# Kernel optimization log

Measured on AMD Instinct MI355X. Metric: run time of the kernel, lower is better.

## Reference

```python
import jax, jax.numpy as jnp
import numpy as np
from jax import lax

WS = 7          # window size
SHIFT = 3       # shift size
HEADS = 16
DIM = 512
NREF = 100
H_IMG = 112
W_IMG = 112
BATCH = 2
HD = DIM // HEADS
SCALE = HD ** (-0.5)
EPS = 1e-5


def _layernorm(x, w, b):
    mu = jnp.mean(x, axis=-1, keepdims=True)
    var = jnp.mean((x - mu) ** 2, axis=-1, keepdims=True)
    return (x - mu) / jnp.sqrt(var + EPS) * w + b


def _rel_pos_index():
    coords = np.stack(np.meshgrid(np.arange(WS), np.arange(WS), indexing='ij'))  # (2,ws,ws)
    cf = coords.reshape(2, -1)
    rel = cf[:, :, None] - cf[:, None, :]
    rel = rel.transpose(1, 2, 0).astype(np.int64)
    rel[..., 0] += WS - 1
    rel[..., 1] += WS - 1
    rel[..., 0] *= 2 * WS - 1
    return rel.sum(-1).reshape(-1)  # (N*N,)

_RPI = _rel_pos_index()


def setup_inputs() -> dict:
    key = jax.random.key(0)
    ks = jax.random.split(key, 16)
    C = DIM
    s = 0.02
    x = jax.random.normal(ks[0], (BATCH, H_IMG * W_IMG, C), jnp.float32)
    x_ref = jax.random.normal(ks[1], (BATCH, NREF, C), jnp.float32)
    # shifted-window attention mask (standard Swin construction)
    img = np.zeros((H_IMG, W_IMG))
    cnt = 0
    for hs in (slice(0, -WS), slice(-WS, -SHIFT), slice(-SHIFT, None)):
        for ws_ in (slice(0, -WS), slice(-WS, -SHIFT), slice(-SHIFT, None)):
            img[hs, ws_] = cnt
            cnt += 1
    mw = img.reshape(H_IMG // WS, WS, W_IMG // WS, WS).transpose(0, 2, 1, 3).reshape(-1, WS * WS)
    am = mw[:, None, :] - mw[:, :, None]
    mask = jnp.asarray(np.where(am != 0, -100.0, 0.0), jnp.float32)  # (nW, N, N)
    return dict(
        x=x, x_ref=x_ref, mask=mask,
        norm1_w=jnp.ones((C,), jnp.float32), norm1_b=jnp.zeros((C,), jnp.float32),
        qkv_w=jax.random.normal(ks[2], (3 * C, C), jnp.float32) * s,
        qkv_b=jnp.zeros((3 * C,), jnp.float32),
        diff_mu=jax.random.normal(ks[3], (1, 1, C), jnp.float32),
        diff_logsigma=jax.random.normal(ks[4], (1, 1, C), jnp.float32) * s,
        rpb_table=jax.random.normal(ks[5], ((2 * WS - 1) ** 2, HEADS), jnp.float32) * s,
        ref_qk_w=jax.random.normal(ks[6], (2 * C, C), jnp.float32) * s,
        ref_qk_b=jnp.zeros((2 * C,), jnp.float32),
        conv_w=jax.random.normal(ks[7], (HEADS, HEADS, 3, 3), jnp.float32) * s,
        conv_b=jnp.zeros((HEADS,), jnp.float32),
        proj_w=jax.random.normal(ks[8], (C, C), jnp.float32) * s,
        proj_b=jnp.zeros((C,), jnp.float32),
        norm2_w=jnp.ones((C,), jnp.float32), norm2_b=jnp.zeros((C,), jnp.float32),
        fc1_w=jax.random.normal(ks[9], (4 * C, C), jnp.float32) * s,
        fc1_b=jnp.zeros((4 * C,), jnp.float32),
        fc2_w=jax.random.normal(ks[10], (C, 4 * C), jnp.float32) * s,
        fc2_b=jnp.zeros((C,), jnp.float32),
        Hh=H_IMG, Ww=W_IMG,
    )


def _window_attention(xw, mask, x_ref, qkv_w, qkv_b, diff_mu, diff_logsigma,
                      rpb_table, ref_qk_w, ref_qk_b, conv_w, conv_b, proj_w, proj_b):
    B_, N, C = xw.shape
    rB = x_ref.shape[0]
    n_win = B_ // rB
    qkv = (xw @ qkv_w.T + qkv_b).reshape(B_, N, 3, HEADS, HD).transpose(2, 0, 3, 1, 4)
    q, k, v = qkv[0], qkv[1], qkv[2]  # (B_, heads, N, hd)
    # reference tokens -> q/v with reparameterized shift/scale
    ref_qk = (x_ref @ ref_qk_w.T + ref_qk_b).reshape(rB, NREF, 2, C).transpose(2, 0, 1, 3)
    ref_q = diff_mu + jnp.exp(diff_logsigma) * ref_qk[0]
    ref_q = ref_q.reshape(rB, NREF, HEADS, HD).transpose(0, 2, 1, 3)
    ref_v = ref_qk[1].reshape(rB, NREF, HEADS, HD).transpose(0, 2, 1, 3)
    ref_k = jnp.repeat(ref_q, n_win, axis=0)  # (B_, heads, nref, hd)
    ref_v = jnp.repeat(ref_v, n_win, axis=0)
    ra = jnp.einsum('bhnd,bhrd->bhnr', q, ref_k)  # (B_, heads, N, nref)
    ra = ra.reshape(rB, n_win, HEADS, N, NREF).transpose(0, 2, 1, 3, 4).reshape(rB, HEADS, n_win * N, NREF)
    # 3 rounds of conv diffusion + layernorm(no affine) + gelu, residual
    for _ in range(3):
        u = lax.conv_general_dilated(ra, conv_w, (1, 1), 'SAME',
                                     dimension_numbers=('NCHW', 'OIHW', 'NCHW'))
        u = u + conv_b[None, :, None, None]
        mu = jnp.mean(u, axis=(-2, -1), keepdims=True)
        var = jnp.mean((u - mu) ** 2, axis=(-2, -1), keepdims=True)
        u = jax.nn.gelu((u - mu) / jnp.sqrt(var + EPS), approximate=False)
        ra = ra + u
    ra = ra.reshape(rB, HEADS, n_win, N, NREF).transpose(0, 2, 1, 3, 4).reshape(B_, HEADS, N, NREF)
    ra = jax.nn.softmax(ra, axis=-1)
    q_new = jnp.einsum('bhnr,bhrd->bhnd', ra, ref_v) * SCALE
    attn = jnp.einsum('bhnd,bhmd->bhnm', q_new, k)
    rpb = rpb_table[_RPI].reshape(N, N, HEADS).transpose(2, 0, 1)  # (heads, N, N)
    attn = attn + rpb[None]
    nW = mask.shape[0]
    attn = attn.reshape(B_ // nW, nW, HEADS, N, N) + mask[None, :, None]
    attn = jax.nn.softmax(attn.reshape(B_, HEADS, N, N), axis=-1)
    out = jnp.einsum('bhnm,bhmd->bhnd', attn, v).transpose(0, 2, 1, 3).reshape(B_, N, C)
    return out @ proj_w.T + proj_b


def reference(x, x_ref, mask, norm1_w, norm1_b, qkv_w, qkv_b, diff_mu, diff_logsigma,
              rpb_table, ref_qk_w, ref_qk_b, conv_w, conv_b, proj_w, proj_b,
              norm2_w, norm2_b, fc1_w, fc1_b, fc2_w, fc2_b, Hh, Ww):
    B, L, C = x.shape
    shortcut = x
    xn = _layernorm(x, norm1_w, norm1_b).reshape(B, Hh, Ww, C)
    # cyclic shift
    sx = jnp.roll(xn, (-SHIFT, -SHIFT), axis=(1, 2))
    # window partition -> (B*nWin, ws*ws, C)
    xw = sx.reshape(B, Hh // WS, WS, Ww // WS, WS, C).transpose(0, 1, 3, 2, 4, 5).reshape(-1, WS * WS, C)
    aw = _window_attention(xw, mask, x_ref, qkv_w, qkv_b, diff_mu, diff_logsigma,
                           rpb_table, ref_qk_w, ref_qk_b, conv_w, conv_b, proj_w, proj_b)
    # window reverse
    sx = aw.reshape(B, Hh // WS, Ww // WS, WS, WS, C).transpose(0, 1, 3, 2, 4, 5).reshape(B, Hh, Ww, C)
    xn = jnp.roll(sx, (SHIFT, SHIFT), axis=(1, 2)).reshape(B, L, C)
    x = shortcut + xn
    h = _layernorm(x, norm2_w, norm2_b)
    h = jax.nn.gelu(h @ fc1_w.T + fc1_b, approximate=False)
    return x + (h @ fc2_w.T + fc2_b)
```

## Files before the change

### kernel.cpp

```cpp
#include <hip/hip_runtime.h>
#include <hip/hip_bf16.h>

typedef __attribute__((ext_vector_type(8))) short short8;
typedef __attribute__((ext_vector_type(8))) unsigned short ushort8;
typedef __attribute__((ext_vector_type(4))) float f32x4;
typedef __attribute__((ext_vector_type(4))) unsigned int u32x4;
typedef __attribute__((ext_vector_type(2))) unsigned int u32x2;

#define DEV __device__ __forceinline__

DEV float gelu_f(float x) { return 0.5f * x * (1.f + erff(x * 0.70710678118654752440f)); }

DEV float bf2f(unsigned short s) {
  unsigned int t = ((unsigned int)s) << 16;
  float f; __builtin_memcpy(&f, &t, 4); return f;
}
DEV unsigned short f2bf(float f) {
  __hip_bfloat16 b = __float2bfloat16(f);
  unsigned short s; __builtin_memcpy(&s, &b, 2); return s;
}

DEV void async_copy16(void* lds, const void* g) {
  __builtin_amdgcn_global_load_lds(
      (const __attribute__((address_space(1))) unsigned int*)g,
      (__attribute__((address_space(3))) unsigned int*)lds, 16, 0, 0);
}

DEV void block_reduce2(float& s, float& s2) {
  __shared__ float red[8];
  int tid = threadIdx.x;
#pragma unroll
  for (int o = 32; o > 0; o >>= 1) { s += __shfl_down(s, o); s2 += __shfl_down(s2, o); }
  if ((tid & 63) == 0) { red[tid >> 6] = s; red[4 + (tid >> 6)] = s2; }
  __syncthreads();
  s  = red[0] + red[1] + red[2] + red[3];
  s2 = red[4] + red[5] + red[6] + red[7];
}

__global__ __launch_bounds__(256) void f2b_kernel(const float* __restrict__ in,
                                                  __hip_bfloat16* __restrict__ o, int n) {
  int i = blockIdx.x * 256 + threadIdx.x;
  if (i < n) o[i] = __float2bfloat16(in[i]);
}

__global__ __launch_bounds__(256) void maskb_kernel(const float* __restrict__ mask,
                                                    unsigned short* __restrict__ maskB) {
  int i = blockIdx.x * 256 + threadIdx.x;
  int m = i % 56, rest = i / 56;
  int n = rest % 49, win = rest / 49;
  unsigned short v = 0;
  if (m < 49) v = f2bf(mask[((size_t)win * 49 + n) * 49 + m]);
  maskB[i] = v;
}

__global__ __launch_bounds__(256) void rpbt_kernel(const float* __restrict__ rpb,
                                                   unsigned short* __restrict__ rpbT) {
  int i = blockIdx.x * 256 + threadIdx.x;
  if (i >= 43904) return;
  int m = i % 56, rest = i / 56;
  int n = rest % 49, h = rest / 49;
  unsigned short v = 0;
  if (m < 49) {
    int rp = (n / 7 - m / 7 + 6) * 13 + (n % 7 - m % 7 + 6);
    v = f2bf(rpb[rp * 16 + h]);
  }
  rpbT[i] = v;
}

__global__ __launch_bounds__(256) void ln1_window_kernel(
    const float* __restrict__ x, const float* __restrict__ w, const float* __restrict__ b,
    __hip_bfloat16* __restrict__ xw) {
  int t = blockIdx.x;
  int b_ = t / 49, n = t % 49;
  int bb = b_ >> 8, win = b_ & 255;
  int wi = win >> 4, wj = win & 15;
  int ii = n / 7, jj = n % 7;
  int sh = (wi * 7 + ii + 3) % 112;
  int sw = (wj * 7 + jj + 3) % 112;
  const float* row = x + ((size_t)bb * 12544 + sh * 112 + sw) * 512;
  int tid = threadIdx.x;
  float v0 = row[tid], v1 = row[tid + 256];
  float s = v0 + v1, s2 = v0 * v0 + v1 * v1;
  block_reduce2(s, s2);
  float mu = s * (1.f / 512.f);
  float rstd = rsqrtf(s2 * (1.f / 512.f) - mu * mu + 1e-5f);
  __hip_bfloat16* orow = xw + (size_t)t * 512;
  orow[tid]       = __float2bfloat16((v0 - mu) * rstd * w[tid] + b[tid]);
  orow[tid + 256] = __float2bfloat16((v1 - mu) * rstd * w[tid + 256] + b[tid + 256]);
}

template <int EPI>
__global__ __launch_bounds__(256) void gemm_bt(
    const __hip_bfloat16* __restrict__ A, const __hip_bfloat16* __restrict__ B,
    const float* __restrict__ bias, float* __restrict__ outF,
    __hip_bfloat16* __restrict__ outB, int M, int N, int K) {
  __shared__ __align__(16) __hip_bfloat16 As[128 * 64];
  __shared__ __align__(16) __hip_bfloat16 Bs[128 * 64];
  int m0 = blockIdx.x * 128, n0 = blockIdx.y * 128;
  int tid = threadIdx.x;
  int wave = tid >> 6, lane = tid & 63;
  int wm = (wave & 1) * 64, wn = (wave >> 1) * 64;
  int lrow = lane & 15, kq = lane >> 4;
  int srow = lane >> 3, scol = (lane & 7) * 8;
  f32x4 acc[4][4] = {};
  for (int k0 = 0; k0 < K; k0 += 64) {
    int rb = wave * 32;
#pragma unroll
    for (int i = 0; i < 4; i++) {
      int row = rb + i * 8 + srow;
      async_copy16(&As[(rb + i * 8) * 64], &A[(size_t)(m0 + row) * K + k0 + scol]);
      async_copy16(&Bs[(rb + i * 8) * 64], &B[(size_t)(n0 + row) * K + k0 + scol]);
    }
    __syncthreads();
#pragma unroll
    for (int ks = 0; ks < 2; ks++) {
      short8 af[4], bf[4];
#pragma unroll
      for (int t = 0; t < 4; t++) {
        af[t] = *reinterpret_cast<const short8*>(&As[(wm + t * 16 + lrow) * 64 + ks * 32 + kq * 8]);
        bf[t] = *reinterpret_cast<const short8*>(&Bs[(wn + t * 16 + lrow) * 64 + ks * 32 + kq * 8]);
      }
#pragma unroll
      for (int tm = 0; tm < 4; tm++)
#pragma unroll
        for (int tn = 0; tn < 4; tn++)
          acc[tm][tn] = __builtin_amdgcn_mfma_f32_16x16x32_bf16(af[tm], bf[tn], acc[tm][tn], 0, 0, 0);
    }
    __syncthreads();
  }
#pragma unroll
  for (int tm = 0; tm < 4; tm++) {
#pragma unroll
    for (int tn = 0; tn < 4; tn++) {
      int col = n0 + wn + tn * 16 + lrow;
      float bv = bias[col];
#pragma unroll
      for (int r = 0; r < 4; r++) {
        int row = m0 + wm + tm * 16 + kq * 4 + r;
        float v = acc[tm][tn][r] + bv;
        size_t o = (size_t)row * N + col;
        if (EPI == 1) outB[o] = __float2bfloat16(v);
        else if (EPI == 2) outB[o] = __float2bfloat16(gelu_f(v));
        else outF[o] += v;
      }
    }
  }
}

__global__ __launch_bounds__(256) void ref_kernel(
    const float* __restrict__ x_ref, const float* __restrict__ w, const float* __restrict__ bias,
    const float* __restrict__ diff_mu, const float* __restrict__ diff_ls,
    unsigned short* __restrict__ refq, unsigned short* __restrict__ refvT) {
  int blk = blockIdx.x;
  int b = blk / 100, r = blk % 100;
  __shared__ float xs[512];
  int tid = threadIdx.x;
  const float* xr = x_ref + (size_t)(b * 100 + r) * 512;
  xs[tid] = xr[tid];
  xs[tid + 256] = xr[tid + 256];
  __syncthreads();
#pragma unroll
  for (int cc = 0; cc < 4; cc++) {
    int c = cc * 256 + tid;
    const float* wr = w + (size_t)c * 512;
    float s = bias[c];
    for (int k = 0; k < 512; k++) s += xs[k] * wr[k];
    if (c < 512) {
      float v = diff_mu[c] + expf(diff_ls[c]) * s;
      int hh = c >> 5, d = c & 31;
      refq[((size_t)(b * 16 + hh) * 100 + r) * 32 + d] = f2bf(v);
    } else {
      int c2 = c - 512, hh = c2 >> 5, d = c2 & 31;
      refvT[(((size_t)b * 16 + hh) * 32 + d) * 100 + r] = f2bf(s);
    }
  }
}

__global__ __launch_bounds__(256) void ra_kernel(
    const __hip_bfloat16* __restrict__ q, const unsigned short* __restrict__ refq,
    __hip_bfloat16* __restrict__ ra) {
  __shared__ __align__(16) unsigned short q_s[64 * 40];
  __shared__ __align__(16) unsigned short rq_s[112 * 40];
  int blk = blockIdx.x;
  int b_ = blk >> 4, h = blk & 15;
  int rb = b_ >> 8, win = b_ & 255;
  int tid = threadIdx.x;
  int wave = tid >> 6, lane = tid & 63;
  int lrow = lane & 15, kq = lane >> 4;
  u32x4 z4 = {};
  const unsigned short* qb = (const unsigned short*)q + (size_t)b_ * 49 * 512 + h * 32;
  for (int i = tid; i < 196; i += 256) {
    int n = i >> 2, c = i & 3;
    *reinterpret_cast<u32x4*>(&q_s[n * 40 + c * 8]) =
        *reinterpret_cast<const u32x4*>(&qb[n * 512 + c * 8]);
  }
  for (int i = tid; i < 60; i += 256) {
    int n = 49 + (i >> 2), c = i & 3;
    *reinterpret_cast<u32x4*>(&q_s[n * 40 + c * 8]) = z4;
  }
  const unsigned short* rqg = refq + (size_t)(rb * 16 + h) * 3200;
  for (int i = tid; i < 400; i += 256) {
    int r = i >> 2, c = i & 3;
    *reinterpret_cast<u32x4*>(&rq_s[r * 40 + c * 8]) =
        *reinterpret_cast<const u32x4*>(&rqg[r * 32 + c * 8]);
  }
  for (int i = tid; i < 48; i += 256) {
    int r = 100 + (i >> 2), c = i & 3;
    *reinterpret_cast<u32x4*>(&rq_s[r * 40 + c * 8]) = z4;
  }
  __syncthreads();
  short8 a = *reinterpret_cast<const short8*>(&q_s[(wave * 16 + lrow) * 40 + kq * 8]);
  unsigned short* ra_base = (unsigned short*)ra + ((size_t)(rb * 16 + h) * 12544 + win * 49) * 100;
  f32x4 zero = {};
#pragma unroll
  for (int nt = 0; nt < 7; nt++) {
    short8 b = *reinterpret_cast<const short8*>(&rq_s[(nt * 16 + lrow) * 40 + kq * 8]);
    f32x4 c = __builtin_amdgcn_mfma_f32_16x16x32_bf16(a, b, zero, 0, 0, 0);
    int col = nt * 16 + lrow;
#pragma unroll
    for (int r = 0; r < 4; r++) {
      int n = wave * 16 + kq * 4 + r;
      if (n < 49 && col < 100) ra_base[n * 100 + col] = f2bf(c[r]);
    }
  }
}

__global__ __launch_bounds__(256) void conv_kernel(
    const __hip_bfloat16* __restrict__ ra_, const float* __restrict__ cw, const float* __restrict__ cb,
    __hip_bfloat16* __restrict__ u_, float* __restrict__ psum, float* __restrict__ psumsq) {
  __shared__ __align__(16) unsigned short in_s[6 * 103 * 24];
  __shared__ __align__(16) unsigned short w_s[16 * 160];
  __shared__ float sred_s[4][16], sred_s2[4][16];
  const unsigned short* ra = (const unsigned short*)ra_;
  unsigned short* u = (unsigned short*)u_;
  int yt = blockIdx.x, bb = blockIdx.y;
  int y0 = yt * 4;
  int tid = threadIdx.x;
  int wave = tid >> 6, lane = tid & 63;
  int lrow = lane & 15, kq = lane >> 4;
  for (int i = tid; i < 2560; i += 256) {
    int co = i / 160, k = i % 160;
    unsigned short v = 0;
    if (k < 144) {
      int ci = k & 15, p = k >> 4;
      v = f2bf(cw[(co * 16 + ci) * 9 + p]);
    }
    w_s[i] = v;
  }
  for (int i = tid; i < 288; i += 256) {
    int ci = i & 15, rem = i >> 4;
    int yl = rem / 3, xs = rem % 3;
    int xl = (xs == 0) ? 0 : (100 + xs);
    in_s[(yl * 103 + xl) * 24 + ci] = 0;
  }
  if (tid < 192) {
    int unit = tid >> 1, par = tid & 1;
    int ci = unit / 6, yl = unit % 6;
    int gy = y0 - 1 + yl;
    bool rv = (gy >= 0 && gy < 12544);
    const unsigned short* rp = ra + (((size_t)bb * 16 + ci) * 12544 + (rv ? gy : 0)) * 100;
    unsigned short* lp = &in_s[(yl * 103 + 1) * 24 + ci];
#pragma unroll 4
    for (int c = par; c < 25; c += 2) {
      u32x2 d = {0u, 0u};
      if (rv) d = *reinterpret_cast<const u32x2*>(&rp[c * 4]);
      lp[(c * 4 + 0) * 24] = (unsigned short)(d[0] & 0xffff);
      lp[(c * 4 + 1) * 24] = (unsigned short)(d[0] >> 16);
      lp[(c * 4 + 2) * 24] = (unsigned short)(d[1] & 0xffff);
      lp[(c * 4 + 3) * 24] = (unsigned short)(d[1] >> 16);
    }
  }
  __syncthreads();

  short8 afr[5];
#pragma unroll
  for (int c = 0; c < 5; c++)
    afr[c] = *reinterpret_cast<const short8*>(&w_s[lrow * 160 + c * 32 + kq * 8]);
  int kqh = kq >> 1, ci0 = (kq & 1) * 8;
  int kyA[5], kxA[5];
#pragma unroll
  for (int c = 0; c < 5; c++) {
    int p = c * 2 + kqh; if (p > 8) p = 0;
    kyA[c] = p / 3; kxA[c] = p % 3;
  }
  float bias_r[4];
#pragma unroll
  for (int r = 0; r < 4; r++) bias_r[r] = cb[kq * 4 + r];
  float s_r[4] = {0.f, 0.f, 0.f, 0.f}, s2_r[4] = {0.f, 0.f, 0.f, 0.f};

  int yl = wave;
  int gy = y0 + yl;
#pragma unroll
  for (int xg = 0; xg < 7; xg++) {
    int px = xg * 16 + lrow;
    int pxc = px < 100 ? px : 99;
    f32x4 acc = {};
#pragma unroll
    for (int c = 0; c < 5; c++) {
      short8 bfrag = *reinterpret_cast<const short8*>(
          &in_s[((yl + kyA[c]) * 103 + pxc + kxA[c]) * 24 + ci0]);
      acc = __builtin_amdgcn_mfma_f32_16x16x32_bf16(afr[c], bfrag, acc, 0, 0, 0);
    }
    bool valid = px < 100;
#pragma unroll
    for (int r = 0; r < 4; r++) {
      float v = acc[r] + bias_r[r];
      if (valid) {
        u[(((size_t)bb * 16 + kq * 4 + r) * 12544 + gy) * 100 + px] = f2bf(v);
        s_r[r] += v; s2_r[r] += v * v;
      }
    }
  }
#pragma unroll
  for (int o = 1; o < 16; o <<= 1)
#pragma unroll
    for (int r = 0; r < 4; r++) { s_r[r] += __shfl_xor(s_r[r], o); s2_r[r] += __shfl_xor(s2_r[r], o); }
  if (lrow == 0)
#pragma unroll
    for (int r = 0; r < 4; r++) { sred_s[wave][kq * 4 + r] = s_r[r]; sred_s2[wave][kq * 4 + r] = s2_r[r]; }
  __syncthreads();
  if (tid < 16) {
    float s  = sred_s[0][tid] + sred_s[1][tid] + sred_s[2][tid] + sred_s[3][tid];
    float s2 = sred_s2[0][tid] + sred_s2[1][tid] + sred_s2[2][tid] + sred_s2[3][tid];
    size_t pi = ((size_t)bb * 3136 + yt) * 16 + tid;
    psum[pi] = s; psumsq[pi] = s2;
  }
}

__global__ __launch_bounds__(256) void conv_stats_kernel(
    const float* __restrict__ psum, const float* __restrict__ psumsq, float* __restrict__ stats) {
  int g = blockIdx.x;
  int bb = g >> 4, co = g & 15;
  int tid = threadIdx.x;
  float s = 0.f, s2 = 0.f;
  for (int t = tid; t < 3136; t += 256) {
    size_t pi = ((size_t)bb * 3136 + t) * 16 + co;
    s += psum[pi];
    s2 += psumsq[pi];
  }
  block_reduce2(s, s2);
  if (tid == 0) {
    const float inv = 1.f / 1254400.f;
    float mu = s * inv;
    float var = s2 * inv - mu * mu;
    stats[g * 2] = mu;
    stats[g * 2 + 1] = rsqrtf(var + 1e-5f);
  }
}

__global__ __launch_bounds__(256) void conv_apply_kernel(
    __hip_bfloat16* __restrict__ ra, const __hip_bfloat16* __restrict__ u,
    const float* __restrict__ stats) {
  const int total8 = 5017600;
  int stride = gridDim.x * 256;
  for (int i = blockIdx.x * 256 + threadIdx.x; i < total8; i += stride) {
    int g = i / 156800;
    float mu = stats[g * 2], rstd = stats[g * 2 + 1];
    ushort8 uu = reinterpret_cast<const ushort8*>(u)[i];
    ushort8 rr = reinterpret_cast<const ushort8*>(ra)[i];
    ushort8 oo;
#pragma unroll
    for (int j = 0; j < 8; j++) {
      float rv = bf2f(rr[j]) + gelu_f((bf2f(uu[j]) - mu) * rstd);
      oo[j] = f2bf(rv);
    }
    reinterpret_cast<ushort8*>(ra)[i] = oo;
  }
}

__global__ __launch_bounds__(256) void attn_kernel(
    const __hip_bfloat16* __restrict__ ra_, const unsigned short* __restrict__ refvT,
    const __hip_bfloat16* __restrict__ kv_, const unsigned short* __restrict__ rpbT,
    const unsigned short* __restrict__ maskB, __hip_bfloat16* __restrict__ att_) {
  __shared__ __align__(16) char smem[36352];
  unsigned short* P1  = (unsigned short*)smem;
  unsigned short* rvT = (unsigned short*)(smem + 17408);
  unsigned short* P2  = (unsigned short*)smem;
  unsigned short* vT  = (unsigned short*)(smem + 9216);
  unsigned short* qn  = (unsigned short*)(smem + 26112);
  unsigned short* kb  = (unsigned short*)(smem + 31232);

  int blk = blockIdx.x;
  int b_ = blk >> 4, h = blk & 15;
  int rb = b_ >> 8, win = b_ & 255;
  int tid = threadIdx.x;
  int wave = tid >> 6, lane = tid & 63;
  int lrow = lane & 15, kq = lane >> 4;
  const unsigned short* ra = (const unsigned short*)ra_;
  const unsigned short* kv = (const unsigned short*)kv_;
  unsigned short* att = (unsigned short*)att_;
  u32x2 zz = {};

  const unsigned short* rab = ra + ((size_t)(rb * 16 + h) * 12544 + win * 49) * 100;
  for (int i = tid; i < 1225; i += 256) {
    int n = i / 25, c = i % 25;
    *reinterpret_cast<u32x2*>(&P1[n * 136 + c * 4]) =
        *reinterpret_cast<const u32x2*>(&rab[n * 100 + c * 4]);
  }
  for (int i = tid; i < 343; i += 256) {
    int n = i / 7, c = i % 7;
    *reinterpret_cast<u32x2*>(&P1[n * 136 + 100 + c * 4]) = zz;
  }
  const unsigned short* rvtg = refvT + (size_t)(rb * 16 + h) * 3200;
  for (int i = tid; i < 800; i += 256) {
    int d = i / 25, c = i % 25;
    *reinterpret_cast<u32x2*>(&rvT[d * 136 + c * 4]) =
        *reinterpret_cast<const u32x2*>(&rvtg[d * 100 + c * 4]);
  }
  for (int i = tid; i < 224; i += 256) {
    int d = i / 7, c = i % 7;
    *reinterpret_cast<u32x2*>(&rvT[d * 136 + 100 + c * 4]) = zz;
  }
  const unsigned short* kvb = kv + (size_t)b_ * 49 * 1024;
  for (int i = tid; i < 196; i += 256) {
    int m = i >> 2, c = i & 3;
    *reinterpret_cast<u32x4*>(&kb[m * 40 + c * 8]) =
        *reinterpret_cast<const u32x4*>(&kvb[m * 1024 + h * 32 + c * 8]);
  }
  __syncthreads();

  if (tid < 196) {
    int n = tid >> 2, q = tid & 3;
    unsigned short* row = P1 + n * 136;
    float mx = -1e30f;
    for (int r = q * 25; r < q * 25 + 25; r++) mx = fmaxf(mx, bf2f(row[r]));
    mx = fmaxf(mx, __shfl_xor(mx, 1));
    mx = fmaxf(mx, __shfl_xor(mx, 2));
    float sm = 0.f;
    for (int r = q * 25; r < q * 25 + 25; r++) {
      float e = __expf(bf2f(row[r]) - mx); sm += e; row[r] = f2bf(e);
    }
    sm += __shfl_xor(sm, 1);
    sm += __shfl_xor(sm, 2);
    float inv = 1.f / sm;
    for (int r = q * 25; r < q * 25 + 25; r++) row[r] = f2bf(bf2f(row[r]) * inv);
  }
  __syncthreads();

  f32x4 acc1[2] = {};
#pragma unroll
  for (int ks = 0; ks < 4; ks++) {
    short8 a = *reinterpret_cast<const short8*>(&P1[(wave * 16 + lrow) * 136 + ks * 32 + kq * 8]);
#pragma unroll
    for (int dt = 0; dt < 2; dt++) {
      short8 b = *reinterpret_cast<const short8*>(&rvT[(dt * 16 + lrow) * 136 + ks * 32 + kq * 8]);
      acc1[dt] = __builtin_amdgcn_mfma_f32_16x16x32_bf16(a, b, acc1[dt], 0, 0, 0);
    }
  }
#pragma unroll
  for (int dt = 0; dt < 2; dt++)
#pragma unroll
    for (int r = 0; r < 4; r++) {
      int n = wave * 16 + kq * 4 + r;
      qn[n * 40 + dt * 16 + lrow] = f2bf(acc1[dt][r] * 0.17677669529663688f);
    }
  __syncthreads();

  for (int i = tid; i < 196; i += 256) {
    int m = i >> 2, dg = (i & 3) * 8;
    ushort8 vv = *reinterpret_cast<const ushort8*>(&kvb[m * 1024 + 512 + h * 32 + dg]);
#pragma unroll
    for (int j = 0; j < 8; j++) vT[(dg + j) * 72 + m] = vv[j];
  }
  for (int i = tid; i < 480; i += 256) vT[(i / 15) * 72 + 49 + i % 15] = 0;

  const unsigned short* bt = maskB + (size_t)win * 2744;
  const unsigned short* rt = rpbT + (size_t)h * 2744;
  short8 aq = *reinterpret_cast<const short8*>(&qn[(wave * 16 + lrow) * 40 + kq * 8]);
  f32x4 zero = {};
  float val[4][4];
#pragma unroll
  for (int mt = 0; mt < 4; mt++) {
    short8 bk = *reinterpret_cast<const short8*>(&kb[(mt * 16 + lrow) * 40 + kq * 8]);
    f32x4 lg = __builtin_amdgcn_mfma_f32_16x16x32_bf16(aq, bk, zero, 0, 0, 0);
    int m = mt * 16 + lrow;
#pragma unroll
    for (int r = 0; r < 4; r++) {
      int n = wave * 16 + kq * 4 + r;
      float v;
      if (m < 49 && n < 49)
        v = lg[r] + bf2f(rt[n * 56 + m]) + bf2f(bt[n * 56 + m]);
      else v = -1e30f;
      val[mt][r] = v;
    }
  }
#pragma unroll
  for (int r = 0; r < 4; r++) {
    float mx = -1e30f;
#pragma unroll
    for (int mt = 0; mt < 4; mt++) mx = fmaxf(mx, val[mt][r]);
    mx = fmaxf(mx, __shfl_xor(mx, 1)); mx = fmaxf(mx, __shfl_xor(mx, 2));
    mx = fmaxf(mx, __shfl_xor(mx, 4)); mx = fmaxf(mx, __shfl_xor(mx, 8));
    float sm = 0.f, e[4];
#pragma unroll
    for (int mt = 0; mt < 4; mt++) { e[mt] = __expf(val[mt][r] - mx); sm += e[mt]; }
    sm += __shfl_xor(sm, 1); sm += __shfl_xor(sm, 2);
    sm += __shfl_xor(sm, 4); sm += __shfl_xor(sm, 8);
    float inv = 1.f / sm;
    int n = wave * 16 + kq * 4 + r;
#pragma unroll
    for (int mt = 0; mt < 4; mt++) P2[n * 72 + mt * 16 + lrow] = f2bf(e[mt] * inv);
  }
  __syncthreads();

  f32x4 acc2[2] = {};
#pragma unroll
  for (int ks = 0; ks < 2; ks++) {
    short8 ap = *reinterpret_cast<const short8*>(&P2[(wave * 16 + lrow) * 72 + ks * 32 + kq * 8]);
#pragma unroll
    for (int dt = 0; dt < 2; dt++) {
      short8 bv = *reinterpret_cast<const short8*>(&vT[(dt * 16 + lrow) * 72 + ks * 32 + kq * 8]);
      acc2[dt] = __builtin_amdgcn_mfma_f32_16x16x32_bf16(ap, bv, acc2[dt], 0, 0, 0);
    }
  }
  unsigned short* ab = att + (size_t)b_ * 49 * 512 + h * 32;
#pragma unroll
  for (int dt = 0; dt < 2; dt++)
#pragma unroll
    for (int r = 0; r < 4; r++) {
      int n = wave * 16 + kq * 4 + r;
      if (n < 49) ab[n * 512 + dt * 16 + lrow] = f2bf(acc2[dt][r]);
    }
}

__global__ __launch_bounds__(256) void resid_ln2_kernel(
    const float* __restrict__ x, const __hip_bfloat16* __restrict__ proj_out,
    const float* __restrict__ w2, const float* __restrict__ b2,
    float* __restrict__ out, __hip_bfloat16* __restrict__ hout) {
  int blk = blockIdx.x;
  int bb = blk / 12544, l = blk % 12544;
  int hh = l / 112, ww = l % 112;
  int hs = (hh + 109) % 112, wsx = (ww + 109) % 112;
  int t = (bb * 256 + (hs / 7) * 16 + (wsx / 7)) * 49 + (hs % 7) * 7 + (wsx % 7);
  const float* xr = x + (size_t)blk * 512;
  const __hip_bfloat16* pr = proj_out + (size_t)t * 512;
  int tid = threadIdx.x;
  float v0 = xr[tid] + __bfloat162float(pr[tid]);
  float v1 = xr[tid + 256] + __bfloat162float(pr[tid + 256]);
  float* orow = out + (size_t)blk * 512;
  orow[tid] = v0;
  orow[tid + 256] = v1;
  float s = v0 + v1, s2 = v0 * v0 + v1 * v1;
  block_reduce2(s, s2);
  float mu = s * (1.f / 512.f);
  float rstd = rsqrtf(s2 * (1.f / 512.f) - mu * mu + 1e-5f);
  __hip_bfloat16* hrow = hout + (size_t)blk * 512;
  hrow[tid]       = __float2bfloat16((v0 - mu) * rstd * w2[tid] + b2[tid]);
  hrow[tid + 256] = __float2bfloat16((v1 - mu) * rstd * w2[tid + 256] + b2[tid + 256]);
}

extern "C" void kernel_launch(void* const* d_in, const int* in_sizes, int n_in,
                              void* d_out, int out_size, void* d_ws, size_t ws_size,
                              hipStream_t stream) {
  const float* x       = (const float*)d_in[0];
  const float* x_ref   = (const float*)d_in[1];
  const float* mask    = (const float*)d_in[2];
  const float* n1w     = (const float*)d_in[3];
  const float* n1b     = (const float*)d_in[4];
  const float* qkv_w   = (const float*)d_in[5];
  const float* qkv_b   = (const float*)d_in[6];
  const float* diff_mu = (const float*)d_in[7];
  const float* diff_ls = (const float*)d_in[8];
  const float* rpb     = (const float*)d_in[9];
  const float* ref_w   = (const float*)d_in[10];
  const float* ref_b   = (const float*)d_in[11];
  const float* conv_w  = (const float*)d_in[12];
  const float* conv_b  = (const float*)d_in[13];
  const float* proj_w  = (const float*)d_in[14];
  const float* proj_b  = (const float*)d_in[15];
  const float* n2w     = (const float*)d_in[16];
  const float* n2b     = (const float*)d_in[17];
  const float* fc1_w   = (const float*)d_in[18];
  const float* fc1_b   = (const float*)d_in[19];
  const float* fc2_w   = (const float*)d_in[20];
  const float* fc2_b   = (const float*)d_in[21];
  float* out = (float*)d_out;

  char* ws = (char*)d_ws;
  size_t off = 0;
  auto alloc = [&](size_t bytes) -> char* {
    char* p = ws + off;
    off += (bytes + 255) & ~(size_t)255;
    return p;
  };
  __hip_bfloat16* wq_bf = (__hip_bfloat16*)alloc(1536ULL * 512 * 2);
  __hip_bfloat16* wp_bf = (__hip_bfloat16*)alloc(512ULL * 512 * 2);
  __hip_bfloat16* w1_bf = (__hip_bfloat16*)alloc(2048ULL * 512 * 2);
  __hip_bfloat16* w2_bf = (__hip_bfloat16*)alloc(512ULL * 2048 * 2);
  unsigned short* refq  = (unsigned short*)alloc(2ULL * 16 * 100 * 32 * 2);
  unsigned short* refvT = (unsigned short*)alloc(2ULL * 16 * 32 * 100 * 2);
  unsigned short* maskB = (unsigned short*)alloc(256ULL * 49 * 56 * 2);
  unsigned short* rpbT  = (unsigned short*)alloc(16ULL * 49 * 56 * 2);
  float* psum  = (float*)alloc(2ULL * 3136 * 16 * 4);
  float* psumq = (float*)alloc(2ULL * 3136 * 16 * 4);
  float* stats = (float*)alloc(64 * 4);
  char* regX  = alloc(25088ULL * 512 * 2);
  char* regQ  = alloc(25088ULL * 512 * 2);
  char* regRA = alloc(2ULL * 16 * 12544 * 100 * 2);
  char* regU  = alloc(2ULL * 16 * 12544 * 100 * 2);

  __hip_bfloat16* xw_bf   = (__hip_bfloat16*)regX;
  __hip_bfloat16* att_bf  = (__hip_bfloat16*)regX;
  __hip_bfloat16* q_bf    = (__hip_bfloat16*)regQ;
  __hip_bfloat16* h_bf    = (__hip_bfloat16*)regQ;
  __hip_bfloat16* ra      = (__hip_bfloat16*)regRA;
  __hip_bfloat16* hg      = (__hip_bfloat16*)regRA;
  __hip_bfloat16* u       = (__hip_bfloat16*)regU;
  __hip_bfloat16* kv_bf   = (__hip_bfloat16*)regU;
  __hip_bfloat16* proj_bf = (__hip_bfloat16*)(regU + 51380224);

  f2b_kernel<<<3072, 256, 0, stream>>>(qkv_w, wq_bf, 786432);
  f2b_kernel<<<1024, 256, 0, stream>>>(proj_w, wp_bf, 262144);
  f2b_kernel<<<4096, 256, 0, stream>>>(fc1_w, w1_bf, 1048576);
  f2b_kernel<<<4096, 256, 0, stream>>>(fc2_w, w2_bf, 1048576);
  maskb_kernel<<<2744, 256, 0, stream>>>(mask, maskB);
  rpbt_kernel<<<172, 256, 0, stream>>>(rpb, rpbT);
  ln1_window_kernel<<<25088, 256, 0, stream>>>(x, n1w, n1b, xw_bf);
  gemm_bt<1><<<dim3(196, 4), 256, 0, stream>>>(xw_bf, wq_bf, qkv_b, nullptr, q_bf,
                                               25088, 512, 512);
  ref_kernel<<<200, 256, 0, stream>>>(x_ref, ref_w, ref_b, diff_mu, diff_ls, refq, refvT);
  ra_kernel<<<8192, 256, 0, stream>>>(q_bf, refq, ra);
  for (int rd = 0; rd < 3; rd++) {
    conv_kernel<<<dim3(3136, 2), 256, 0, stream>>>(ra, conv_w, conv_b, u, psum, psumq);
    conv_stats_kernel<<<32, 256, 0, stream>>>(psum, psumq, stats);
    conv_apply_kernel<<<4096, 256, 0, stream>>>(ra, u, stats);
  }
  gemm_bt<1><<<dim3(196, 8), 256, 0, stream>>>(xw_bf, wq_bf + 512 * 512, qkv_b + 512,
                                               nullptr, kv_bf, 25088, 1024, 512);
  attn_kernel<<<8192, 256, 0, stream>>>(ra, refvT, kv_bf, rpbT, maskB, att_bf);
  gemm_bt<1><<<dim3(196, 4), 256, 0, stream>>>(att_bf, wp_bf, proj_b, nullptr, proj_bf,
                                               25088, 512, 512);
  resid_ln2_kernel<<<25088, 256, 0, stream>>>(x, proj_bf, n2w, n2b, out, h_bf);
  for (int ch = 0; ch < 2; ch++) {
    const __hip_bfloat16* hA = h_bf + (size_t)ch * 12544 * 512;
    gemm_bt<2><<<dim3(98, 16), 256, 0, stream>>>(hA, w1_bf, fc1_b, nullptr, hg,
                                                 12544, 2048, 512);
    gemm_bt<3><<<dim3(98, 4), 256, 0, stream>>>(hg, w2_bf, fc2_b,
                                                out + (size_t)ch * 12544 * 512, nullptr,
                                                12544, 512, 2048);
  }
}
```

Before: 1.187 ms.

## Fuse final conv residual-GELU into attention kernel and defer softmax normalization

The last conv_apply pass is skipped. Its residual plus GELU on the normalized conv output is instead computed inside the attention kernel as the ref-attention tile is loaded. Because u must stay live until then, kv gets its own buffer when the workspace is large enough, with the old aliasing kept as a fallback. The ref softmax now keeps values in registers and folds the 1/sum into the scale applied after the MFMA, which drops one LDS read-modify-write pass. The cost is an extra global read of u inside attention and more workspace memory.

Measured after the change: 1.185 ms. No clear change (-0.2%).

```diff
diff --git a/kernel.cpp b/kernel.cpp
--- a/kernel.cpp
+++ b/kernel.cpp
@@ -368,17 +368,20 @@
   }
 }
 
+template <int FUSE>
 __global__ __launch_bounds__(256) void attn_kernel(
-    const __hip_bfloat16* __restrict__ ra_, const unsigned short* __restrict__ refvT,
+    const __hip_bfloat16* __restrict__ ra_, const __hip_bfloat16* __restrict__ u_,
+    const float* __restrict__ stats, const unsigned short* __restrict__ refvT,
     const __hip_bfloat16* __restrict__ kv_, const unsigned short* __restrict__ rpbT,
     const unsigned short* __restrict__ maskB, __hip_bfloat16* __restrict__ att_) {
-  __shared__ __align__(16) char smem[36352];
+  __shared__ __align__(16) char smem[36608];
   unsigned short* P1  = (unsigned short*)smem;
   unsigned short* rvT = (unsigned short*)(smem + 17408);
   unsigned short* P2  = (unsigned short*)smem;
   unsigned short* vT  = (unsigned short*)(smem + 9216);
   unsigned short* qn  = (unsigned short*)(smem + 26112);
   unsigned short* kb  = (unsigned short*)(smem + 31232);
+  float* lsum         = (float*)(smem + 36352);
 
   int blk = blockIdx.x;
   int b_ = blk >> 4, h = blk & 15;
@@ -387,15 +390,38 @@
   int wave = tid >> 6, lane = tid & 63;
   int lrow = lane & 15, kq = lane >> 4;
   const unsigned short* ra = (const unsigned short*)ra_;
+  const unsigned short* ug = (const unsigned short*)u_;
   const unsigned short* kv = (const unsigned short*)kv_;
   unsigned short* att = (unsigned short*)att_;
   u32x2 zz = {};
 
-  const unsigned short* rab = ra + ((size_t)(rb * 16 + h) * 12544 + win * 49) * 100;
+  if (tid < 64) lsum[tid] = 1.0f;
+  float mu = 0.f, rstd = 0.f;
+  if (FUSE) { mu = stats[(rb * 16 + h) * 2]; rstd = stats[(rb * 16 + h) * 2 + 1]; }
+
+  const size_t tile_off = ((size_t)(rb * 16 + h) * 12544 + win * 49) * 100;
+  const unsigned short* rab = ra + tile_off;
+  const unsigned short* uab = ug + tile_off;
   for (int i = tid; i < 1225; i += 256) {
     int n = i / 25, c = i % 25;
-    *reinterpret_cast<u32x2*>(&P1[n * 136 + c * 4]) =
-        *reinterpret_cast<const u32x2*>(&rab[n * 100 + c * 4]);
+    u32x2 rv = *reinterpret_cast<const u32x2*>(&rab[n * 100 + c * 4]);
+    if (FUSE) {
+      u32x2 uv = *reinterpret_cast<const u32x2*>(&uab[n * 100 + c * 4]);
+      unsigned short rr4[4] = {(unsigned short)(rv[0] & 0xffff), (unsigned short)(rv[0] >> 16),
+                               (unsigned short)(rv[1] & 0xffff), (unsigned short)(rv[1] >> 16)};
+      unsigned short uu4[4] = {(unsigned short)(uv[0] & 0xffff), (unsigned short)(uv[0] >> 16),
+                               (unsigned short)(uv[1] & 0xffff), (unsigned short)(uv[1] >> 16)};
+      unsigned short o4[4];
+#pragma unroll
+      for (int j = 0; j < 4; j++)
+        o4[j] = f2bf(bf2f(rr4[j]) + gelu_f((bf2f(uu4[j]) - mu) * rstd));
+      u32x2 w;
+      w[0] = (unsigned int)o4[0] | ((unsigned int)o4[1] << 16);
+      w[1] = (unsigned int)o4[2] | ((unsigned int)o4[3] << 16);
+      *reinterpret_cast<u32x2*>(&P1[n * 136 + c * 4]) = w;
+    } else {
+      *reinterpret_cast<u32x2*>(&P1[n * 136 + c * 4]) = rv;
+    }
   }
   for (int i = tid; i < 343; i += 256) {
     int n = i / 7, c = i % 7;
@@ -421,19 +447,23 @@
 
   if (tid < 196) {
     int n = tid >> 2, q = tid & 3;
-    unsigned short* row = P1 + n * 136;
+    unsigned short* row = P1 + n * 136 + q * 25;
+    float e[25];
+#pragma unroll
+    for (int r = 0; r < 25; r++) e[r] = bf2f(row[r]);
     float mx = -1e30f;
-    for (int r = q * 25; r < q * 25 + 25; r++) mx = fmaxf(mx, bf2f(row[r]));
+#pragma unroll
+    for (int r = 0; r < 25; r++) mx = fmaxf(mx, e[r]);
     mx = fmaxf(mx, __shfl_xor(mx, 1));
     mx = fmaxf(mx, __shfl_xor(mx, 2));
     float sm = 0.f;
-    for (int r = q * 25; r < q * 25 + 25; r++) {
-      float e = __expf(bf2f(row[r]) - mx); sm += e; row[r] = f2bf(e);
-    }
+#pragma unroll
+    for (int r = 0; r < 25; r++) { e[r] = __expf(e[r] - mx); sm += e[r]; }
     sm += __shfl_xor(sm, 1);
     sm += __shfl_xor(sm, 2);
-    float inv = 1.f / sm;
-    for (int r = q * 25; r < q * 25 + 25; r++) row[r] = f2bf(bf2f(row[r]) * inv);
+#pragma unroll
+    for (int r = 0; r < 25; r++) row[r] = f2bf(e[r]);
+    if (q == 0) lsum[n] = sm;
   }
   __syncthreads();
 
@@ -447,12 +477,16 @@
       acc1[dt] = __builtin_amdgcn_mfma_f32_16x16x32_bf16(a, b, acc1[dt], 0, 0, 0);
     }
   }
+  float invl[4];
+#pragma unroll
+  for (int r = 0; r < 4; r++)
+    invl[r] = 0.17677669529663688f / lsum[wave * 16 + kq * 4 + r];
 #pragma unroll
   for (int dt = 0; dt < 2; dt++)
 #pragma unroll
     for (int r = 0; r < 4; r++) {
       int n = wave * 16 + kq * 4 + r;
-      qn[n * 40 + dt * 16 + lrow] = f2bf(acc1[dt][r] * 0.17677669529663688f);
+      qn[n * 40 + dt * 16 + lrow] = f2bf(acc1[dt][r] * invl[r]);
     }
   __syncthreads();
 
@@ -606,8 +640,12 @@
   __hip_bfloat16* ra      = (__hip_bfloat16*)regRA;
   __hip_bfloat16* hg      = (__hip_bfloat16*)regRA;
   __hip_bfloat16* u       = (__hip_bfloat16*)regU;
-  __hip_bfloat16* kv_bf   = (__hip_bfloat16*)regU;
   __hip_bfloat16* proj_bf = (__hip_bfloat16*)(regU + 51380224);
+
+  const size_t kv_bytes = 25088ULL * 1024 * 2;
+  bool fused = (ws_size >= off + kv_bytes);
+  __hip_bfloat16* kv_bf = fused ? (__hip_bfloat16*)alloc(kv_bytes)
+                                : (__hip_bfloat16*)regU;
 
   f2b_kernel<<<3072, 256, 0, stream>>>(qkv_w, wq_bf, 786432);
   f2b_kernel<<<1024, 256, 0, stream>>>(proj_w, wp_bf, 262144);
@@ -623,11 +661,15 @@
   for (int rd = 0; rd < 3; rd++) {
     conv_kernel<<<dim3(3136, 2), 256, 0, stream>>>(ra, conv_w, conv_b, u, psum, psumq);
     conv_stats_kernel<<<32, 256, 0, stream>>>(psum, psumq, stats);
-    conv_apply_kernel<<<4096, 256, 0, stream>>>(ra, u, stats);
+    if (rd < 2 || !fused)
+      conv_apply_kernel<<<4096, 256, 0, stream>>>(ra, u, stats);
   }
   gemm_bt<1><<<dim3(196, 8), 256, 0, stream>>>(xw_bf, wq_bf + 512 * 512, qkv_b + 512,
                                                nullptr, kv_bf, 25088, 1024, 512);
-  attn_kernel<<<8192, 256, 0, stream>>>(ra, refvT, kv_bf, rpbT, maskB, att_bf);
+  if (fused)
+    attn_kernel<1><<<8192, 256, 0, stream>>>(ra, u, stats, refvT, kv_bf, rpbT, maskB, att_bf);
+  else
+    attn_kernel<0><<<8192, 256, 0, stream>>>(ra, u, stats, refvT, kv_bf, rpbT, maskB, att_bf);
   gemm_bt<1><<<dim3(196, 4), 256, 0, stream>>>(att_bf, wp_bf, proj_b, nullptr, proj_bf,
                                                25088, 512, 512);
   resid_ln2_kernel<<<25088, 256, 0, stream>>>(x, proj_bf, n2w, n2b, out, h_bf);
```
